# Performance work log

Hardware: AMD Instinct MI355X
Metric: run time of the kernel (lower is better)

Reference implementation:

```python
import jax, jax.numpy as jnp
import numpy as np

B, T, N, R, I = 32, 512, 1024, 4, 8
DT = 0.1
G = 0.9


def setup_inputs() -> dict:
    key = jax.random.key(0)
    k1, k2, k3, k4, k5 = jax.random.split(key, 5)
    inputs = jax.random.normal(k1, (B, T, I, 1), dtype=jnp.float32)
    f = jax.random.normal(k2, (B, T, R, 1), dtype=jnp.float32)
    J = jax.random.normal(k3, (B, N, N), dtype=jnp.float32) * (G / np.sqrt(N))
    wIn = jax.random.normal(k4, (B, N, I), dtype=jnp.float32)
    m = jax.random.normal(k5, (B, N, R), dtype=jnp.float32)
    return {"inputs": inputs, "f": f, "J": J, "wIn": wIn, "m": m}


def _run(inputs, f, J, wIn, m):
    dt = DT
    dtype = inputs.dtype
    x0 = jnp.zeros((B, N, 1), dtype)
    n0 = jnp.zeros((B, N, R), dtype)
    P0 = jnp.tile(jnp.eye(N, dtype=dtype)[None] / 10.0, (B, 1, 1))

    def step(carry, t_in):
        x, P, n = carry
        u, f_t = t_in                               # u: (B,I,1), f_t: (B,R,1)
        # recurrence (r, z computed from PRE-update x, matching original)
        r = jnp.tanh(x)                             # (B,N,1)
        z = jnp.einsum('bnk,bns->bks', n, r)        # n^T @ r -> (B,R,1)
        x_new = (1.0 - dt) * x + dt * (J @ r + m @ z + wIn @ u)
        # RLS update (uses r from pre-update x)
        Pr = P @ r                                  # (B,N,1)
        rPr = jnp.sum(r * Pr, axis=1, keepdims=True)  # r^T P r -> (B,1,1)
        c = 1.0 / (1.0 + rPr)                       # scalar per batch
        P_new = P - c * (Pr @ jnp.swapaxes(Pr, -1, -2))
        err = z - f_t                               # (B,R,1)
        n_new = n - c * (Pr @ jnp.swapaxes(err, -1, -2))
        return (x_new, P_new, n_new), (x_new, z)

    u_seq = jnp.swapaxes(inputs, 0, 1)              # (T,B,I,1)
    f_seq = jnp.swapaxes(f, 0, 1)                   # (T,B,R,1)
    _, (xs, zs) = jax.lax.scan(step, (x0, P0, n0), (u_seq, f_seq))
    all_x = jnp.swapaxes(xs, 0, 1)                  # (B,T,N,1)
    all_z = jnp.swapaxes(zs, 0, 1)                  # (B,T,R,1)
    return all_x, all_z


def reference(inputs, f, J, wIn, m):
    return _run(inputs, f, J, wIn, m)
```

## Files before the change

### kernel.cpp

```cpp
#include <hip/hip_runtime.h>
#include <hip/hip_bf16.h>

#define BB 32
#define TT 512
#define NN 1024
#define RR 4
#define II 8
#define DT_C 0.1f

#define BPB 32
#define GRID (BB * BPB)

#define NBLK 32
#define ROWS (NN / NBLK)
#define VBLK 16

typedef __attribute__((ext_vector_type(8))) unsigned short ushort8v;

__device__ __forceinline__ float bf2f(unsigned short u) {
    union { unsigned int ui; float f; } cv;
    cv.ui = ((unsigned int)u) << 16;
    return cv.f;
}
__device__ __forceinline__ unsigned short f2bf_rne(float x) {
    union { float f; unsigned int ui; } cv; cv.f = x;
    unsigned int u = cv.ui;
    u += 0x7FFFu + ((u >> 16) & 1u);
    return (unsigned short)(u >> 16);
}
__device__ __forceinline__ float wave_reduce(float v) {
    #pragma unroll
    for (int off = 32; off; off >>= 1) v += __shfl_down(v, off, 64);
    return v;
}

__device__ __forceinline__ void llc_ld16x2(const void* p0, const void* p1,
                                           uint4& a, uint4& b) {
    asm volatile("global_load_dwordx4 %0, %2, off sc0 sc1\n\t"
                 "global_load_dwordx4 %1, %3, off sc0 sc1\n\t"
                 "s_waitcnt vmcnt(0)"
                 : "=&v"(a), "=&v"(b) : "v"(p0), "v"(p1) : "memory");
}
__device__ __forceinline__ uint4 llc_ld16(const void* p) {
    uint4 r;
    asm volatile("global_load_dwordx4 %0, %1, off sc0 sc1\n\ts_waitcnt vmcnt(0)"
                 : "=&v"(r) : "v"(p) : "memory");
    return r;
}
__device__ __forceinline__ float llc_ldf(const float* p) {
    float r;
    asm volatile("global_load_dword %0, %1, off sc0 sc1\n\ts_waitcnt vmcnt(0)"
                 : "=&v"(r) : "v"(p) : "memory");
    return r;
}
__device__ __forceinline__ void llc_ld4f(const float* p0, const float* p1,
                                         const float* p2, const float* p3,
                                         float& a, float& b, float& c, float& d) {
    asm volatile("global_load_dword %0, %4, off sc0 sc1\n\t"
                 "global_load_dword %1, %5, off sc0 sc1\n\t"
                 "global_load_dword %2, %6, off sc0 sc1\n\t"
                 "global_load_dword %3, %7, off sc0 sc1\n\t"
                 "s_waitcnt vmcnt(0)"
                 : "=&v"(a), "=&v"(b), "=&v"(c), "=&v"(d)
                 : "v"(p0), "v"(p1), "v"(p2), "v"(p3) : "memory");
}
__device__ __forceinline__ void llc_stf(float* p, float v) {
    asm volatile("global_store_dword %0, %1, off sc0 sc1" :: "v"(p), "v"(v) : "memory");
}
__device__ __forceinline__ void llc_st16b(unsigned short* p, unsigned short v) {
    asm volatile("global_store_short %0, %1, off sc0 sc1"
                 :: "v"(p), "v"((unsigned)v) : "memory");
}

__device__ __forceinline__ void accum8(float& acc, const uint4 q, const float* ap) {
    acc = fmaf(bf2f((unsigned short)(q.x & 0xffffu)), ap[0], acc);
    acc = fmaf(bf2f((unsigned short)(q.x >> 16)),     ap[1], acc);
    acc = fmaf(bf2f((unsigned short)(q.y & 0xffffu)), ap[2], acc);
    acc = fmaf(bf2f((unsigned short)(q.y >> 16)),     ap[3], acc);
    acc = fmaf(bf2f((unsigned short)(q.z & 0xffffu)), ap[4], acc);
    acc = fmaf(bf2f((unsigned short)(q.z >> 16)),     ap[5], acc);
    acc = fmaf(bf2f((unsigned short)(q.w & 0xffffu)), ap[6], acc);
    acc = fmaf(bf2f((unsigned short)(q.w >> 16)),     ap[7], acc);
}


__global__ __launch_bounds__(256) void k_convJ(const float* __restrict__ J,
                                               unsigned short* __restrict__ Jp) {
    const int row = blockIdx.x;
    const int tid = threadIdx.x;
    __shared__ float rowsh[NN];
    const float4* __restrict__ src = (const float4*)(J + (size_t)row * NN);
    float4* dst4 = (float4*)rowsh;
    for (int k = tid; k < NN / 4; k += 256) dst4[k] = src[k];
    __syncthreads();
    const int o0 = tid * 4;
    unsigned short out[4];
    #pragma unroll
    for (int j = 0; j < 4; ++j) {
        const int o = o0 + j;
        const int l = (o >> 3) & 63, g = o >> 9, e = o & 7;
        out[j] = f2bf_rne(rowsh[l + 64 * (8 * g + e)]);
    }
    uint2 w;
    w.x = (unsigned int)out[0] | ((unsigned int)out[1] << 16);
    w.y = (unsigned int)out[2] | ((unsigned int)out[3] << 16);
    *(uint2*)(Jp + (size_t)row * NN + o0) = w;
}

__device__ __forceinline__ void batch_barrier(unsigned* cnt, unsigned* gen,
                                              unsigned expect) {
    asm volatile("s_waitcnt vmcnt(0) lgkmcnt(0)" ::: "memory");
    __syncthreads();
    if (threadIdx.x == 0) {
        unsigned old = __hip_atomic_fetch_add(cnt, 1u, __ATOMIC_RELAXED,
                                              __HIP_MEMORY_SCOPE_AGENT);
        if (old == BPB - 1u) {
            __hip_atomic_store(cnt, 0u, __ATOMIC_RELAXED, __HIP_MEMORY_SCOPE_AGENT);
            asm volatile("s_waitcnt vmcnt(0)" ::: "memory");
            __hip_atomic_fetch_add(gen, 1u, __ATOMIC_RELAXED, __HIP_MEMORY_SCOPE_AGENT);
        } else {
            while (__hip_atomic_load(gen, __ATOMIC_RELAXED, __HIP_MEMORY_SCOPE_AGENT)
                   < expect)
                __builtin_amdgcn_s_sleep(2);
        }
    }
    __syncthreads();
}

#define ACC2(q, base) \
    acc = fmaf(bf2f((unsigned short)((q) & 0xffffu)), r_sh[(base)], acc); \
    acc = fmaf(bf2f((unsigned short)((q) >> 16)), r_sh[(base) + 64], acc);

__global__ __launch_bounds__(256, 4) void k_persist(
    const unsigned short* __restrict__ Jp,
    unsigned short* __restrict__ V1,
    unsigned short* __restrict__ V2,
    float* __restrict__ x,
    float* __restrict__ abuf,
    float* __restrict__ part,
    float* __restrict__ part2,
    unsigned* __restrict__ cnt, unsigned* __restrict__ gen,
    const float* __restrict__ m, const float* __restrict__ wIn,
    const float* __restrict__ inputs, const float* __restrict__ f,
    float* __restrict__ outx, float* __restrict__ outz)
{
    const int bid = blockIdx.x;
    const int b = (bid & 7) * 4 + (bid >> 8);
    const int k = (bid >> 3) & 31;
    const int tid = threadIdx.x, lane = tid & 63, wave = tid >> 6;
    const int row_loc = tid >> 3, sub = tid & 7;
    const int i_loc = k * 32 + row_loc;

    __shared__ float r_sh[NN];
    __shared__ float a_sh[TT];
    __shared__ float Jr_sh[32];
    __shared__ float zred[32][4];
    __shared__ float red_neg[4], red_rr[4];
    __shared__ float sgred[33];
    __shared__ float zr2[128];
    __shared__ float zsh[RR], esh[RR], ush[II], csh[2];

    unsigned* mycnt = cnt + b * 32;
    unsigned* mygen = gen + b * 32;
    unsigned bar = 0;

    float4 nrow = {0.f, 0.f, 0.f, 0.f};
    float xreg = 0.f;

    for (int t = 0; t < TT; ++t) {
        {
            float x0, x1, x2, x3;
            const float* xb = x + b * NN + tid;
            llc_ld4f(xb, xb + 256, xb + 512, xb + 768, x0, x1, x2, x3);
            r_sh[tid]       = tanhf(x0);
            r_sh[tid + 256] = tanhf(x1);
            r_sh[tid + 512] = tanhf(x2);
            r_sh[tid + 768] = tanhf(x3);
        }
        __syncthreads();

        for (int rr = wave; rr < 32; rr += 4) {
            const int row = k * 32 + rr;
            const ushort8v* __restrict__ Jrow =
                (const ushort8v*)(Jp + ((size_t)b * NN + row) * NN);
            const ushort8v j0 = Jrow[lane];
            const ushort8v j1 = Jrow[64 + lane];
            float acc = 0.f;
            #pragma unroll
            for (int e = 0; e < 8; ++e)
                acc = fmaf(bf2f(j0[e]), r_sh[lane + 64 * e], acc);
            #pragma unroll
            for (int e = 0; e < 8; ++e)
                acc = fmaf(bf2f(j1[e]), r_sh[lane + 512 + 64 * e], acc);
            acc = wave_reduce(acc);
            if (lane == 0) Jr_sh[rr] = acc;
        }

        if (sub == 0) {
            const float rv = r_sh[i_loc];
            zred[row_loc][0] = nrow.x * rv;
            zred[row_loc][1] = nrow.y * rv;
            zred[row_loc][2] = nrow.z * rv;
            zred[row_loc][3] = nrow.w * rv;
        }

        float negsum = 0.f;
        for (int s = k + 32 * wave; s < t; s += 128) {
            const unsigned short* colp = V1 + ((size_t)b * TT + s) * NN;
            uint4 q0, q1;
            llc_ld16x2(colp + lane * 8, colp + (64 + lane) * 8, q0, q1);
            float acc = 0.f;
            ACC2(q0.x, lane);       ACC2(q0.y, lane + 128);
            ACC2(q0.z, lane + 256); ACC2(q0.w, lane + 384);
            ACC2(q1.x, lane + 512); ACC2(q1.y, lane + 640);
            ACC2(q1.z, lane + 768); ACC2(q1.w, lane + 896);
            acc = wave_reduce(acc);
            if (lane == 0) {
                llc_stf(abuf + b * TT + s, acc);
                negsum = fmaf(-acc, acc, negsum);
            }
        }
        if (lane == 0) red_neg[wave] = negsum;

        if (k == 0) {
            float p = 0.f;
            for (int j = tid; j < NN; j += 256) p = fmaf(r_sh[j], r_sh[j], p);
            p = wave_reduce(p);
            if (lane == 0) red_rr[wave] = p;
        }
        __syncthreads();
        if (tid < 4) {
            float zp = 0.f;
            #pragma unroll
            for (int kk = 0; kk < 32; ++kk) zp += zred[kk][tid];
            llc_stf(part2 + b * 128 + k * 4 + tid, zp);
        }
        if (tid == 0)
            llc_stf(part + b * 64 + k,
                    red_neg[0] + red_neg[1] + red_neg[2] + red_neg[3]);
        if (k == 0 && tid == 0)
            llc_stf(part + b * 64 + 32,
                    0.1f * (red_rr[0] + red_rr[1] + red_rr[2] + red_rr[3]));

        batch_barrier(mycnt, mygen, ++bar);

        const int nv4 = (t + 3) >> 2;
        if (tid < nv4) {
            union { uint4 u; float4 fv; } cv;
            cv.u = llc_ld16(abuf + b * TT + tid * 4);
            const int s0 = tid * 4;
            a_sh[s0]     = (s0     < t) ? cv.fv.x : 0.f;
            a_sh[s0 + 1] = (s0 + 1 < t) ? cv.fv.y : 0.f;
            a_sh[s0 + 2] = (s0 + 2 < t) ? cv.fv.z : 0.f;
            a_sh[s0 + 3] = (s0 + 3 < t) ? cv.fv.w : 0.f;
        }
        for (int j2 = nv4 * 4 + tid; j2 < TT; j2 += 256) a_sh[j2] = 0.f;
        if (tid < 33) sgred[tid] = llc_ldf(part + b * 64 + tid);
        if (tid >= 64 && tid < 192) zr2[tid - 64] = llc_ldf(part2 + b * 128 + (tid - 64));
        if (tid >= 192 && tid < 192 + II)
            ush[tid - 192] = inputs[((size_t)b * TT + t) * II + (tid - 192)];
        __syncthreads();
        if (tid == 0) {
            float sg = 0.f;
            #pragma unroll
            for (int q2 = 0; q2 < 33; ++q2) sg += sgred[q2];
            const float c = 1.f / (1.f + sg);
            csh[0] = c; csh[1] = sqrtf(c);
        }
        if (tid < 4) {
            float zq = 0.f;
            #pragma unroll
            for (int kk = 0; kk < 32; ++kk) zq += zr2[kk * 4 + tid];
            zsh[tid] = zq;
            esh[tid] = zq - f[((size_t)b * TT + t) * RR + tid];
        }
        __syncthreads();

        const unsigned short* vrow = V2 + ((size_t)b * NN + i_loc) * TT;
        const int nj = (t + 63) >> 6;
        float acc = 0.f;
        int j2 = 0;
        for (; j2 + 2 <= nj; j2 += 2) {
            uint4 qa, qb;
            const int o0 = j2 * 64 + sub * 8, o1 = o0 + 64;
            llc_ld16x2(vrow + o0, vrow + o1, qa, qb);
            accum8(acc, qa, a_sh + o0);
            accum8(acc, qb, a_sh + o1);
        }
        if (j2 < nj) {
            const int o0 = j2 * 64 + sub * 8;
            uint4 qa = llc_ld16(vrow + o0);
            accum8(acc, qa, a_sh + o0);
        }
        acc += __shfl_down(acc, 4, 8);
        acc += __shfl_down(acc, 2, 8);
        acc += __shfl_down(acc, 1, 8);

        if (sub == 0) {
            const float c = csh[0], sq = csh[1];
            const float pr = 0.1f * r_sh[i_loc] - acc;
            const unsigned short hv = f2bf_rne(sq * pr);
            const int ge = i_loc >> 6;
            const int o = (ge >> 3) * 512 + (i_loc & 63) * 8 + (ge & 7);
            llc_st16b(V1 + ((size_t)b * TT + t) * NN + o, hv);
            llc_st16b(V2 + ((size_t)b * NN + i_loc) * TT + t, hv);

            float accx = Jr_sh[row_loc];
            const float4 mv = *(const float4*)(m + ((size_t)b * NN + i_loc) * RR);
            accx = fmaf(mv.x, zsh[0], accx); accx = fmaf(mv.y, zsh[1], accx);
            accx = fmaf(mv.z, zsh[2], accx); accx = fmaf(mv.w, zsh[3], accx);
            const float4* __restrict__ wp =
                (const float4*)(wIn + ((size_t)b * NN + i_loc) * II);
            const float4 w0 = wp[0], w1 = wp[1];
            accx = fmaf(w0.x, ush[0], accx); accx = fmaf(w0.y, ush[1], accx);
            accx = fmaf(w0.z, ush[2], accx); accx = fmaf(w0.w, ush[3], accx);
            accx = fmaf(w1.x, ush[4], accx); accx = fmaf(w1.y, ush[5], accx);
            accx = fmaf(w1.z, ush[6], accx); accx = fmaf(w1.w, ush[7], accx);
            const float xn = (1.0f - DT_C) * xreg + DT_C * accx;
            xreg = xn;
            llc_stf(x + b * NN + i_loc, xn);
            outx[((size_t)b * TT + t) * NN + i_loc] = xn;

            const float cpr = c * pr;
            nrow.x = fmaf(-cpr, esh[0], nrow.x);
            nrow.y = fmaf(-cpr, esh[1], nrow.y);
            nrow.z = fmaf(-cpr, esh[2], nrow.z);
            nrow.w = fmaf(-cpr, esh[3], nrow.w);
        }
        if (k == 0 && tid < RR) outz[((size_t)b * TT + t) * RR + tid] = zsh[tid];

        batch_barrier(mycnt, mygen, ++bar);
    }
}


__global__ __launch_bounds__(256) void kA_fb(
    const float* __restrict__ x, const unsigned short* __restrict__ Jp,
    const unsigned short* __restrict__ Vp, const float* __restrict__ nmat,
    float* __restrict__ r_out, float* __restrict__ a_out,
    float* __restrict__ Jr, float* __restrict__ zbuf,
    float* __restrict__ part, int t)
{
    const int b   = blockIdx.x / (NBLK + VBLK);
    const int blk = blockIdx.x % (NBLK + VBLK);
    const int tid = threadIdx.x, lane = tid & 63, wave = tid >> 6;

    __shared__ float r_sh[NN];
    __shared__ float red_sh[4];

    for (int j = tid; j < NN; j += 256) {
        const float rv = tanhf(x[b * NN + j]);
        r_sh[j] = rv;
        if (blk == 0) r_out[b * NN + j] = rv;
    }
    __syncthreads();

    if (blk < NBLK) {
        for (int rr = wave; rr < ROWS; rr += 4) {
            const int row = blk * ROWS + rr;
            const ushort8v* __restrict__ Jrow =
                (const ushort8v*)(Jp + ((size_t)b * NN + row) * NN);
            const ushort8v jv0 = Jrow[lane];
            const ushort8v jv1 = Jrow[64 + lane];
            float acc = 0.0f;
            #pragma unroll
            for (int e = 0; e < 8; ++e) acc = fmaf(bf2f(jv0[e]), r_sh[lane + 64 * e], acc);
            #pragma unroll
            for (int e = 0; e < 8; ++e) acc = fmaf(bf2f(jv1[e]), r_sh[lane + 512 + 64 * e], acc);
            acc = wave_reduce(acc);
            if (lane == 0) Jr[b * NN + row] = acc;
        }
        if (blk == 0) {
            float p = 0.0f;
            for (int j = tid; j < NN; j += 256) p = fmaf(r_sh[j], r_sh[j], p);
            p = wave_reduce(p);
            if (lane == 0) red_sh[wave] = p;
            __syncthreads();
            if (tid == 0)
                part[b * 72 + 64] = 0.1f * (red_sh[0] + red_sh[1] + red_sh[2] + red_sh[3]);
            if (wave < RR) {
                float acc = 0.0f;
                for (int i2 = lane; i2 < NN; i2 += 64)
                    acc = fmaf(nmat[((size_t)b * NN + i2) * RR + wave], r_sh[i2], acc);
                acc = wave_reduce(acc);
                if (lane == 0) zbuf[b * RR + wave] = acc;
            }
        }
    } else {
        const int wid = (blk - NBLK) * 4 + wave;
        float negsum = 0.0f;
        for (int s = wid; s < t; s += 64) {
            const ushort8v* __restrict__ col =
                (const ushort8v*)(Vp + ((size_t)b * TT + s) * NN);
            const ushort8v vv0 = col[lane];
            const ushort8v vv1 = col[64 + lane];
            float acc = 0.0f;
            #pragma unroll
            for (int e = 0; e < 8; ++e) acc = fmaf(bf2f(vv0[e]), r_sh[lane + 64 * e], acc);
            #pragma unroll
            for (int e = 0; e < 8; ++e) acc = fmaf(bf2f(vv1[e]), r_sh[lane + 512 + 64 * e], acc);
            acc = wave_reduce(acc);
            if (lane == 0) {
                a_out[b * TT + s] = acc;
                negsum = fmaf(-acc, acc, negsum);
            }
        }
        if (lane == 0) part[b * 72 + wid] = negsum;
    }
}

__global__ __launch_bounds__(256) void kB_fb(
    unsigned short* __restrict__ Vp, const float* __restrict__ r,
    const float* __restrict__ a, const float* __restrict__ Jr,
    const float* __restrict__ zbuf, const float* __restrict__ part,
    float* __restrict__ x, float* __restrict__ nmat,
    const float* __restrict__ m, const float* __restrict__ wIn,
    const float* __restrict__ inputs, const float* __restrict__ f,
    float* __restrict__ outx, float* __restrict__ outz, int t)
{
    const int b   = blockIdx.x >> 3;
    const int tb  = blockIdx.x & 7;
    const int tid = threadIdx.x;
    const int pl    = tid & 63;
    const int slice = tid >> 6;

    __shared__ float a_sh[TT];
    __shared__ float ps[4][128];
    __shared__ float zsh[RR], esh[RR], ush[II];

    for (int s = tid; s < t; s += 256) a_sh[s] = a[b * TT + s];
    if (tid < RR) {
        const float zv = zbuf[b * RR + tid];
        zsh[tid] = zv;
        esh[tid] = zv - f[((size_t)b * TT + t) * RR + tid];
    }
    if (tid >= 64 && tid < 64 + II)
        ush[tid - 64] = inputs[((size_t)b * TT + t) * II + (tid - 64)];
    __syncthreads();

    const int p0 = (tb * 64 + pl) * 2;
    const unsigned short* __restrict__ Vb = Vp + (size_t)b * TT * NN;

    const int s_begin = (t * slice) >> 2;
    const int s_end   = (t * (slice + 1)) >> 2;
    float acc0 = 0.0f, acc1 = 0.0f;
    #pragma unroll 4
    for (int s = s_begin; s < s_end; ++s) {
        const unsigned int w = *(const unsigned int*)(Vb + (size_t)s * NN + p0);
        const float av = a_sh[s];
        acc0 = fmaf(bf2f((unsigned short)(w & 0xFFFFu)), av, acc0);
        acc1 = fmaf(bf2f((unsigned short)(w >> 16)), av, acc1);
    }
    ps[slice][pl * 2]     = acc0;
    ps[slice][pl * 2 + 1] = acc1;
    __syncthreads();

    if (slice == 0) {
        const int l = (p0 >> 3) & 63, g = p0 >> 9, e = p0 & 7;
        const int i0 = l + 64 * (8 * g + e);
        const int i1 = i0 + 64;
        const float s0 = ps[0][pl * 2] + ps[1][pl * 2] + ps[2][pl * 2] + ps[3][pl * 2];
        const float s1 = ps[0][pl * 2 + 1] + ps[1][pl * 2 + 1] + ps[2][pl * 2 + 1] + ps[3][pl * 2 + 1];

        float sg = 0.0f;
        #pragma unroll
        for (int q = 0; q < 65; ++q) sg += part[b * 72 + q];
        const float c  = 1.0f / (1.0f + sg);
        const float sq = sqrtf(c);

        const float pr0 = 0.1f * r[b * NN + i0] - s0;
        const float pr1 = 0.1f * r[b * NN + i1] - s1;

        unsigned int wv = (unsigned int)f2bf_rne(sq * pr0) |
                          ((unsigned int)f2bf_rne(sq * pr1) << 16);
        *(unsigned int*)(Vp + ((size_t)b * TT + t) * NN + p0) = wv;

        #pragma unroll
        for (int which = 0; which < 2; ++which) {
            const int   i  = which ? i1 : i0;
            const float pr = which ? pr1 : pr0;
            float acc = Jr[b * NN + i];
            const float4 mv = *(const float4*)(m + ((size_t)b * NN + i) * RR);
            acc = fmaf(mv.x, zsh[0], acc); acc = fmaf(mv.y, zsh[1], acc);
            acc = fmaf(mv.z, zsh[2], acc); acc = fmaf(mv.w, zsh[3], acc);
            const float4* __restrict__ wp = (const float4*)(wIn + ((size_t)b * NN + i) * II);
            const float4 w0 = wp[0], w1 = wp[1];
            acc = fmaf(w0.x, ush[0], acc); acc = fmaf(w0.y, ush[1], acc);
            acc = fmaf(w0.z, ush[2], acc); acc = fmaf(w0.w, ush[3], acc);
            acc = fmaf(w1.x, ush[4], acc); acc = fmaf(w1.y, ush[5], acc);
            acc = fmaf(w1.z, ush[6], acc); acc = fmaf(w1.w, ush[7], acc);
            const float xo = x[b * NN + i];
            const float xn = (1.0f - DT_C) * xo + DT_C * acc;
            x[b * NN + i] = xn;
            outx[((size_t)b * TT + t) * NN + i] = xn;

            float4* __restrict__ np = (float4*)(nmat + ((size_t)b * NN + i) * RR);
            float4 nv = *np;
            const float cpr = c * pr;
            nv.x = fmaf(-cpr, esh[0], nv.x); nv.y = fmaf(-cpr, esh[1], nv.y);
            nv.z = fmaf(-cpr, esh[2], nv.z); nv.w = fmaf(-cpr, esh[3], nv.w);
            *np = nv;
        }
    }
    if (tb == 0 && tid < RR) outz[((size_t)b * TT + t) * RR + tid] = zsh[tid];
}

extern "C" void kernel_launch(void* const* d_in, const int* in_sizes, int n_in,
                              void* d_out, int out_size, void* d_ws, size_t ws_size,
                              hipStream_t stream) {
    const float* inputs = (const float*)d_in[0];
    const float* f      = (const float*)d_in[1];
    const float* J      = (const float*)d_in[2];
    const float* wIn    = (const float*)d_in[3];
    const float* m      = (const float*)d_in[4];

    float* outx = (float*)d_out;
    float* outz = outx + (size_t)BB * TT * NN;

    char* ws = (char*)d_ws;
    size_t off = 0;
    unsigned short* Jp = (unsigned short*)(ws + off); off += (size_t)BB * NN * NN * 2;
    unsigned short* V1 = (unsigned short*)(ws + off); off += (size_t)BB * TT * NN * 2;
    unsigned short* V2 = (unsigned short*)(ws + off); off += (size_t)BB * NN * TT * 2;
    float* x      = (float*)(ws + off); off += (size_t)BB * NN * 4;
    float* abuf   = (float*)(ws + off); off += (size_t)BB * TT * 4;
    float* part   = (float*)(ws + off); off += (size_t)BB * 64 * 4;
    float* part2  = (float*)(ws + off); off += (size_t)BB * 128 * 4;
    unsigned* cnt = (unsigned*)(ws + off); off += (size_t)BB * 32 * 4;
    unsigned* gen = (unsigned*)(ws + off); off += (size_t)BB * 32 * 4;
    float* nm     = (float*)(ws + off); off += (size_t)BB * NN * RR * 4;
    float* rbuf   = (float*)(ws + off); off += (size_t)BB * NN * 4;
    float* Jrb    = (float*)(ws + off); off += (size_t)BB * NN * 4;
    float* zb     = (float*)(ws + off); off += (size_t)BB * RR * 4 + 256;
    float* part72 = (float*)(ws + off); off += (size_t)BB * 72 * 4;

    hipMemsetAsync(x,   0, (size_t)BB * NN * sizeof(float), stream);
    hipMemsetAsync(nm,  0, (size_t)BB * NN * RR * sizeof(float), stream);
    hipMemsetAsync(cnt, 0, (size_t)BB * 32 * sizeof(unsigned), stream);
    hipMemsetAsync(gen, 0, (size_t)BB * 32 * sizeof(unsigned), stream);

    k_convJ<<<BB * NN, 256, 0, stream>>>(J, Jp);

    void* kargs[] = {
        (void*)&Jp, (void*)&V1, (void*)&V2, (void*)&x,
        (void*)&abuf, (void*)&part, (void*)&part2, (void*)&cnt, (void*)&gen,
        (void*)&m, (void*)&wIn, (void*)&inputs, (void*)&f,
        (void*)&outx, (void*)&outz
    };
    hipError_t rc = hipLaunchCooperativeKernel((const void*)k_persist,
                                               dim3(GRID), dim3(256),
                                               kargs, 0, stream);
    if (rc != hipSuccess) {
        for (int t = 0; t < TT; ++t) {
            kA_fb<<<BB * (NBLK + VBLK), 256, 0, stream>>>(x, Jp, V1, nm, rbuf, abuf,
                                                          Jrb, zb, part72, t);
            kB_fb<<<BB * 8, 256, 0, stream>>>(V1, rbuf, abuf, Jrb, zb, part72,
                                              x, nm, m, wIn, inputs, f, outx, outz, t);
        }
    }
}
```

Measured before the change: 9.451 ms.

## Keep J slice in registers and V panel in LDS, reorder per-step partials

Each persistent block now loads its bf16 slice of J into 64 registers per thread once, instead of re-reading J rows from global memory every timestep. The low-rank V factors for the block's 32 rows are held in shared memory rather than in two global buffers. The projection partials for the next step are computed locally and exchanged through small global buffers. The intent is to remove the per-step global traffic for J and V. In exchange, register and LDS use rises sharply, which may lower occupancy or cause spills, and the barrier sequence per step is rearranged to use two batch barriers.

```diff
diff --git a/kernel.cpp b/kernel.cpp
--- a/kernel.cpp
+++ b/kernel.cpp
@@ -18,14 +18,17 @@
 typedef __attribute__((ext_vector_type(8))) unsigned short ushort8v;
 
 __device__ __forceinline__ float bf2f(unsigned short u) {
-    union { unsigned int ui; float f; } cv;
-    cv.ui = ((unsigned int)u) << 16;
-    return cv.f;
+    union { unsigned int ui; float f; } cv; cv.ui = ((unsigned int)u) << 16; return cv.f;
+}
+__device__ __forceinline__ float bf2f_lo(unsigned int u) {
+    union { unsigned int ui; float f; } cv; cv.ui = u << 16; return cv.f;
+}
+__device__ __forceinline__ float bf2f_hi(unsigned int u) {
+    union { unsigned int ui; float f; } cv; cv.ui = u & 0xffff0000u; return cv.f;
 }
 __device__ __forceinline__ unsigned short f2bf_rne(float x) {
     union { float f; unsigned int ui; } cv; cv.f = x;
-    unsigned int u = cv.ui;
-    u += 0x7FFFu + ((u >> 16) & 1u);
+    unsigned int u = cv.ui; u += 0x7FFFu + ((u >> 16) & 1u);
     return (unsigned short)(u >> 16);
 }
 __device__ __forceinline__ float wave_reduce(float v) {
@@ -34,13 +37,6 @@
     return v;
 }
 
-__device__ __forceinline__ void llc_ld16x2(const void* p0, const void* p1,
-                                           uint4& a, uint4& b) {
-    asm volatile("global_load_dwordx4 %0, %2, off sc0 sc1\n\t"
-                 "global_load_dwordx4 %1, %3, off sc0 sc1\n\t"
-                 "s_waitcnt vmcnt(0)"
-                 : "=&v"(a), "=&v"(b) : "v"(p0), "v"(p1) : "memory");
-}
 __device__ __forceinline__ uint4 llc_ld16(const void* p) {
     uint4 r;
     asm volatile("global_load_dwordx4 %0, %1, off sc0 sc1\n\ts_waitcnt vmcnt(0)"
@@ -53,58 +49,40 @@
                  : "=&v"(r) : "v"(p) : "memory");
     return r;
 }
-__device__ __forceinline__ void llc_ld4f(const float* p0, const float* p1,
-                                         const float* p2, const float* p3,
-                                         float& a, float& b, float& c, float& d) {
-    asm volatile("global_load_dword %0, %4, off sc0 sc1\n\t"
-                 "global_load_dword %1, %5, off sc0 sc1\n\t"
-                 "global_load_dword %2, %6, off sc0 sc1\n\t"
-                 "global_load_dword %3, %7, off sc0 sc1\n\t"
+__device__ __forceinline__ void llc_ldf2(const float* p0, const float* p1,
+                                         float& a, float& b) {
+    asm volatile("global_load_dword %0, %2, off sc0 sc1\n\t"
+                 "global_load_dword %1, %3, off sc0 sc1\n\t"
                  "s_waitcnt vmcnt(0)"
-                 : "=&v"(a), "=&v"(b), "=&v"(c), "=&v"(d)
-                 : "v"(p0), "v"(p1), "v"(p2), "v"(p3) : "memory");
+                 : "=&v"(a), "=&v"(b) : "v"(p0), "v"(p1) : "memory");
 }
 __device__ __forceinline__ void llc_stf(float* p, float v) {
     asm volatile("global_store_dword %0, %1, off sc0 sc1" :: "v"(p), "v"(v) : "memory");
 }
-__device__ __forceinline__ void llc_st16b(unsigned short* p, unsigned short v) {
-    asm volatile("global_store_short %0, %1, off sc0 sc1"
-                 :: "v"(p), "v"((unsigned)v) : "memory");
-}
-
-__device__ __forceinline__ void accum8(float& acc, const uint4 q, const float* ap) {
-    acc = fmaf(bf2f((unsigned short)(q.x & 0xffffu)), ap[0], acc);
-    acc = fmaf(bf2f((unsigned short)(q.x >> 16)),     ap[1], acc);
-    acc = fmaf(bf2f((unsigned short)(q.y & 0xffffu)), ap[2], acc);
-    acc = fmaf(bf2f((unsigned short)(q.y >> 16)),     ap[3], acc);
-    acc = fmaf(bf2f((unsigned short)(q.z & 0xffffu)), ap[4], acc);
-    acc = fmaf(bf2f((unsigned short)(q.z >> 16)),     ap[5], acc);
-    acc = fmaf(bf2f((unsigned short)(q.w & 0xffffu)), ap[6], acc);
-    acc = fmaf(bf2f((unsigned short)(q.w >> 16)),     ap[7], acc);
-}
-
-
-__global__ __launch_bounds__(256) void k_convJ(const float* __restrict__ J,
-                                               unsigned short* __restrict__ Jp) {
-    const int row = blockIdx.x;
-    const int tid = threadIdx.x;
-    __shared__ float rowsh[NN];
-    const float4* __restrict__ src = (const float4*)(J + (size_t)row * NN);
-    float4* dst4 = (float4*)rowsh;
-    for (int k = tid; k < NN / 4; k += 256) dst4[k] = src[k];
-    __syncthreads();
-    const int o0 = tid * 4;
-    unsigned short out[4];
+__device__ __forceinline__ void llc_st8(float* p, float a, float b) {
+    float2 v; v.x = a; v.y = b;
+    asm volatile("global_store_dwordx2 %0, %1, off sc0 sc1" :: "v"(p), "v"(v) : "memory");
+}
+
+__global__ __launch_bounds__(256) void k_convJl(const float* __restrict__ J,
+                                                unsigned int* __restrict__ Jl) {
+    const int b = blockIdx.x >> 5, k = blockIdx.x & 31;
+    const int w = threadIdx.x >> 6, l = threadIdx.x & 63;
+    unsigned int* dst = Jl + ((((size_t)(b * 32 + k) * 4 + w) * 64 + l) * 64);
     #pragma unroll
-    for (int j = 0; j < 4; ++j) {
-        const int o = o0 + j;
-        const int l = (o >> 3) & 63, g = o >> 9, e = o & 7;
-        out[j] = f2bf_rne(rowsh[l + 64 * (8 * g + e)]);
-    }
-    uint2 w;
-    w.x = (unsigned int)out[0] | ((unsigned int)out[1] << 16);
-    w.y = (unsigned int)out[2] | ((unsigned int)out[3] << 16);
-    *(uint2*)(Jp + (size_t)row * NN + o0) = w;
+    for (int j = 0; j < 8; ++j) {
+        const int row = k * 32 + w * 8 + j;
+        const float* __restrict__ Jrow = J + ((size_t)b * NN + row) * NN;
+        unsigned int out[8];
+        #pragma unroll
+        for (int e2 = 0; e2 < 8; ++e2) {
+            const int c0 = l + 128 * e2;
+            out[e2] = (unsigned int)f2bf_rne(Jrow[c0]) |
+                      ((unsigned int)f2bf_rne(Jrow[c0 + 64]) << 16);
+        }
+        *(uint4*)(dst + j * 8)     = make_uint4(out[0], out[1], out[2], out[3]);
+        *(uint4*)(dst + j * 8 + 4) = make_uint4(out[4], out[5], out[6], out[7]);
+    }
 }
 
 __device__ __forceinline__ void batch_barrier(unsigned* cnt, unsigned* gen,
@@ -127,18 +105,14 @@
     __syncthreads();
 }
 
-#define ACC2(q, base) \
-    acc = fmaf(bf2f((unsigned short)((q) & 0xffffu)), r_sh[(base)], acc); \
-    acc = fmaf(bf2f((unsigned short)((q) >> 16)), r_sh[(base) + 64], acc);
-
 __global__ __launch_bounds__(256, 4) void k_persist(
-    const unsigned short* __restrict__ Jp,
-    unsigned short* __restrict__ V1,
-    unsigned short* __restrict__ V2,
-    float* __restrict__ x,
+    const unsigned int* __restrict__ Jl,
+    float* __restrict__ rbuf,
     float* __restrict__ abuf,
-    float* __restrict__ part,
-    float* __restrict__ part2,
+    float* __restrict__ pa,
+    float* __restrict__ sqpart,
+    float* __restrict__ r2part,
+    float* __restrict__ zpart,
     unsigned* __restrict__ cnt, unsigned* __restrict__ gen,
     const float* __restrict__ m, const float* __restrict__ wIn,
     const float* __restrict__ inputs, const float* __restrict__ f,
@@ -151,159 +125,157 @@
     const int row_loc = tid >> 3, sub = tid & 7;
     const int i_loc = k * 32 + row_loc;
 
+    __shared__ unsigned short V_lds[32][512];
     __shared__ float r_sh[NN];
     __shared__ float a_sh[TT];
+    __shared__ float r_next[32];
     __shared__ float Jr_sh[32];
+    __shared__ float r2sh[32];
     __shared__ float zred[32][4];
-    __shared__ float red_neg[4], red_rr[4];
-    __shared__ float sgred[33];
-    __shared__ float zr2[128];
-    __shared__ float zsh[RR], esh[RR], ush[II], csh[2];
+    __shared__ float red4[4][16];
+    __shared__ float csh[2], zsh[RR], esh[RR], ush[II];
 
     unsigned* mycnt = cnt + b * 32;
     unsigned* mygen = gen + b * 32;
     unsigned bar = 0;
 
+    unsigned int jreg[64];
+    {
+        const uint4* jp = (const uint4*)(Jl +
+            ((((size_t)(b * 32 + k) * 4 + wave) * 64 + lane) * 64));
+        #pragma unroll
+        for (int q = 0; q < 16; ++q) {
+            uint4 v = jp[q];
+            jreg[q * 4] = v.x; jreg[q * 4 + 1] = v.y;
+            jreg[q * 4 + 2] = v.z; jreg[q * 4 + 3] = v.w;
+        }
+    }
+    {
+        unsigned long long* vz = (unsigned long long*)&V_lds[0][0];
+        for (int q = tid; q < 32 * 512 / 4; q += 256) vz[q] = 0ull;
+    }
     float4 nrow = {0.f, 0.f, 0.f, 0.f};
     float xreg = 0.f;
+    if (sub == 0) llc_stf(rbuf + b * NN + i_loc, 0.f);
+    if (tid < 4)  llc_stf(zpart + b * 128 + k * 4 + tid, 0.f);
+    if (tid == 4) llc_stf(r2part + b * 32 + k, 0.f);
+    batch_barrier(mycnt, mygen, ++bar);
 
     for (int t = 0; t < TT; ++t) {
         {
-            float x0, x1, x2, x3;
-            const float* xb = x + b * NN + tid;
-            llc_ld4f(xb, xb + 256, xb + 512, xb + 768, x0, x1, x2, x3);
-            r_sh[tid]       = tanhf(x0);
-            r_sh[tid + 256] = tanhf(x1);
-            r_sh[tid + 512] = tanhf(x2);
-            r_sh[tid + 768] = tanhf(x3);
-        }
+            const int s_off = tid & 15, kk = tid >> 4;
+            const int s = k * 16 + s_off;
+            float v = 0.f;
+            if (s < t) {
+                float v0, v1;
+                llc_ldf2(pa + ((size_t)b * 32 + kk) * TT + s,
+                         pa + ((size_t)b * 32 + kk + 16) * TT + s, v0, v1);
+                v = v0 + v1;
+            }
+            v += __shfl_down(v, 32, 64);
+            v += __shfl_down(v, 16, 64);
+            if ((tid & 63) < 16) red4[wave][s_off] = v;
+            __syncthreads();
+            if (tid < 16) {
+                float a = red4[0][tid] + red4[1][tid] + red4[2][tid] + red4[3][tid];
+                const int s2 = k * 16 + tid;
+                float sq = 0.f;
+                if (s2 < t) { llc_stf(abuf + b * TT + s2, a); sq = a * a; }
+                sq += __shfl_down(sq, 8, 16);
+                sq += __shfl_down(sq, 4, 16);
+                sq += __shfl_down(sq, 2, 16);
+                sq += __shfl_down(sq, 1, 16);
+                if (tid == 0) llc_stf(sqpart + b * 32 + k, sq);
+            }
+        }
+        batch_barrier(mycnt, mygen, ++bar);
+
+        {
+            union { uint4 u; float4 fv; } cv;
+            cv.u = llc_ld16(rbuf + b * NN + tid * 4);
+            *(float4*)&r_sh[tid * 4] = cv.fv;
+        }
+        if (tid < 128) {
+            const int s0 = tid * 4;
+            if (s0 < t) {
+                union { uint4 u; float4 fv; } cv;
+                cv.u = llc_ld16(abuf + b * TT + s0);
+                a_sh[s0]     = cv.fv.x;
+                a_sh[s0 + 1] = (s0 + 1 < t) ? cv.fv.y : 0.f;
+                a_sh[s0 + 2] = (s0 + 2 < t) ? cv.fv.z : 0.f;
+                a_sh[s0 + 3] = (s0 + 3 < t) ? cv.fv.w : 0.f;
+            } else {
+                *(float4*)&a_sh[s0] = make_float4(0.f, 0.f, 0.f, 0.f);
+            }
+        }
+        if (wave == 0) {
+            float v = (lane < 32) ? 0.1f * llc_ldf(r2part + b * 32 + lane)
+                                  : -llc_ldf(sqpart + b * 32 + (lane - 32));
+            v = wave_reduce(v);
+            if (lane == 0) {
+                const float c = 1.f / (1.f + v);
+                csh[0] = c; csh[1] = sqrtf(c);
+            }
+        } else if (wave == 1) {
+            float v0, v1;
+            llc_ldf2(zpart + b * 128 + lane, zpart + b * 128 + 64 + lane, v0, v1);
+            float v = v0 + v1;
+            v += __shfl_down(v, 32, 64);
+            v += __shfl_down(v, 16, 64);
+            v += __shfl_down(v, 8, 64);
+            v += __shfl_down(v, 4, 64);
+            if (lane < RR) {
+                zsh[lane] = v;
+                esh[lane] = v - f[((size_t)b * TT + t) * RR + lane];
+                if (k == 0) outz[((size_t)b * TT + t) * RR + lane] = v;
+            }
+        }
+        if (tid >= 128 && tid < 128 + II)
+            ush[tid - 128] = inputs[((size_t)b * TT + t) * II + (tid - 128)];
         __syncthreads();
 
-        for (int rr = wave; rr < 32; rr += 4) {
-            const int row = k * 32 + rr;
-            const ushort8v* __restrict__ Jrow =
-                (const ushort8v*)(Jp + ((size_t)b * NN + row) * NN);
-            const ushort8v j0 = Jrow[lane];
-            const ushort8v j1 = Jrow[64 + lane];
-            float acc = 0.f;
-            #pragma unroll
-            for (int e = 0; e < 8; ++e)
-                acc = fmaf(bf2f(j0[e]), r_sh[lane + 64 * e], acc);
-            #pragma unroll
-            for (int e = 0; e < 8; ++e)
-                acc = fmaf(bf2f(j1[e]), r_sh[lane + 512 + 64 * e], acc);
-            acc = wave_reduce(acc);
-            if (lane == 0) Jr_sh[rr] = acc;
-        }
-
-        if (sub == 0) {
-            const float rv = r_sh[i_loc];
-            zred[row_loc][0] = nrow.x * rv;
-            zred[row_loc][1] = nrow.y * rv;
-            zred[row_loc][2] = nrow.z * rv;
-            zred[row_loc][3] = nrow.w * rv;
-        }
-
-        float negsum = 0.f;
-        for (int s = k + 32 * wave; s < t; s += 128) {
-            const unsigned short* colp = V1 + ((size_t)b * TT + s) * NN;
-            uint4 q0, q1;
-            llc_ld16x2(colp + lane * 8, colp + (64 + lane) * 8, q0, q1);
-            float acc = 0.f;
-            ACC2(q0.x, lane);       ACC2(q0.y, lane + 128);
-            ACC2(q0.z, lane + 256); ACC2(q0.w, lane + 384);
-            ACC2(q1.x, lane + 512); ACC2(q1.y, lane + 640);
-            ACC2(q1.z, lane + 768); ACC2(q1.w, lane + 896);
-            acc = wave_reduce(acc);
-            if (lane == 0) {
-                llc_stf(abuf + b * TT + s, acc);
-                negsum = fmaf(-acc, acc, negsum);
-            }
-        }
-        if (lane == 0) red_neg[wave] = negsum;
-
-        if (k == 0) {
-            float p = 0.f;
-            for (int j = tid; j < NN; j += 256) p = fmaf(r_sh[j], r_sh[j], p);
-            p = wave_reduce(p);
-            if (lane == 0) red_rr[wave] = p;
-        }
+        float accJ[8] = {0.f, 0.f, 0.f, 0.f, 0.f, 0.f, 0.f, 0.f};
+        #pragma unroll
+        for (int e2 = 0; e2 < 8; ++e2) {
+            const float rv0 = r_sh[lane + 128 * e2];
+            const float rv1 = r_sh[lane + 128 * e2 + 64];
+            #pragma unroll
+            for (int j = 0; j < 8; ++j) {
+                const unsigned int w = jreg[j * 8 + e2];
+                accJ[j] = fmaf(bf2f_lo(w), rv0, accJ[j]);
+                accJ[j] = fmaf(bf2f_hi(w), rv1, accJ[j]);
+            }
+        }
+        #pragma unroll
+        for (int j = 0; j < 8; ++j) {
+            float v = wave_reduce(accJ[j]);
+            if (lane == 0) Jr_sh[wave * 8 + j] = v;
+        }
+
+        float accp = 0.f;
+        for (int mm = 0; mm * 64 < t; ++mm) {
+            const int s0 = mm * 64 + sub * 8;
+            const ushort8v vv = *(const ushort8v*)&V_lds[row_loc][s0];
+            const float4 a0 = *(const float4*)&a_sh[s0];
+            const float4 a1 = *(const float4*)&a_sh[s0 + 4];
+            accp = fmaf(bf2f(vv[0]), a0.x, accp);
+            accp = fmaf(bf2f(vv[1]), a0.y, accp);
+            accp = fmaf(bf2f(vv[2]), a0.z, accp);
+            accp = fmaf(bf2f(vv[3]), a0.w, accp);
+            accp = fmaf(bf2f(vv[4]), a1.x, accp);
+            accp = fmaf(bf2f(vv[5]), a1.y, accp);
+            accp = fmaf(bf2f(vv[6]), a1.z, accp);
+            accp = fmaf(bf2f(vv[7]), a1.w, accp);
+        }
+        accp += __shfl_down(accp, 4, 8);
+        accp += __shfl_down(accp, 2, 8);
+        accp += __shfl_down(accp, 1, 8);
         __syncthreads();
-        if (tid < 4) {
-            float zp = 0.f;
-            #pragma unroll
-            for (int kk = 0; kk < 32; ++kk) zp += zred[kk][tid];
-            llc_stf(part2 + b * 128 + k * 4 + tid, zp);
-        }
-        if (tid == 0)
-            llc_stf(part + b * 64 + k,
-                    red_neg[0] + red_neg[1] + red_neg[2] + red_neg[3]);
-        if (k == 0 && tid == 0)
-            llc_stf(part + b * 64 + 32,
-                    0.1f * (red_rr[0] + red_rr[1] + red_rr[2] + red_rr[3]));
-
-        batch_barrier(mycnt, mygen, ++bar);
-
-        const int nv4 = (t + 3) >> 2;
-        if (tid < nv4) {
-            union { uint4 u; float4 fv; } cv;
-            cv.u = llc_ld16(abuf + b * TT + tid * 4);
-            const int s0 = tid * 4;
-            a_sh[s0]     = (s0     < t) ? cv.fv.x : 0.f;
-            a_sh[s0 + 1] = (s0 + 1 < t) ? cv.fv.y : 0.f;
-            a_sh[s0 + 2] = (s0 + 2 < t) ? cv.fv.z : 0.f;
-            a_sh[s0 + 3] = (s0 + 3 < t) ? cv.fv.w : 0.f;
-        }
-        for (int j2 = nv4 * 4 + tid; j2 < TT; j2 += 256) a_sh[j2] = 0.f;
-        if (tid < 33) sgred[tid] = llc_ldf(part + b * 64 + tid);
-        if (tid >= 64 && tid < 192) zr2[tid - 64] = llc_ldf(part2 + b * 128 + (tid - 64));
-        if (tid >= 192 && tid < 192 + II)
-            ush[tid - 192] = inputs[((size_t)b * TT + t) * II + (tid - 192)];
-        __syncthreads();
-        if (tid == 0) {
-            float sg = 0.f;
-            #pragma unroll
-            for (int q2 = 0; q2 < 33; ++q2) sg += sgred[q2];
-            const float c = 1.f / (1.f + sg);
-            csh[0] = c; csh[1] = sqrtf(c);
-        }
-        if (tid < 4) {
-            float zq = 0.f;
-            #pragma unroll
-            for (int kk = 0; kk < 32; ++kk) zq += zr2[kk * 4 + tid];
-            zsh[tid] = zq;
-            esh[tid] = zq - f[((size_t)b * TT + t) * RR + tid];
-        }
-        __syncthreads();
-
-        const unsigned short* vrow = V2 + ((size_t)b * NN + i_loc) * TT;
-        const int nj = (t + 63) >> 6;
-        float acc = 0.f;
-        int j2 = 0;
-        for (; j2 + 2 <= nj; j2 += 2) {
-            uint4 qa, qb;
-            const int o0 = j2 * 64 + sub * 8, o1 = o0 + 64;
-            llc_ld16x2(vrow + o0, vrow + o1, qa, qb);
-            accum8(acc, qa, a_sh + o0);
-            accum8(acc, qb, a_sh + o1);
-        }
-        if (j2 < nj) {
-            const int o0 = j2 * 64 + sub * 8;
-            uint4 qa = llc_ld16(vrow + o0);
-            accum8(acc, qa, a_sh + o0);
-        }
-        acc += __shfl_down(acc, 4, 8);
-        acc += __shfl_down(acc, 2, 8);
-        acc += __shfl_down(acc, 1, 8);
 
         if (sub == 0) {
             const float c = csh[0], sq = csh[1];
-            const float pr = 0.1f * r_sh[i_loc] - acc;
-            const unsigned short hv = f2bf_rne(sq * pr);
-            const int ge = i_loc >> 6;
-            const int o = (ge >> 3) * 512 + (i_loc & 63) * 8 + (ge & 7);
-            llc_st16b(V1 + ((size_t)b * TT + t) * NN + o, hv);
-            llc_st16b(V2 + ((size_t)b * NN + i_loc) * TT + t, hv);
+            const float pr = 0.1f * r_sh[i_loc] - accp;
+            V_lds[row_loc][t] = f2bf_rne(sq * pr);
 
             float accx = Jr_sh[row_loc];
             const float4 mv = *(const float4*)(m + ((size_t)b * NN + i_loc) * RR);
@@ -318,7 +290,6 @@
             accx = fmaf(w1.z, ush[6], accx); accx = fmaf(w1.w, ush[7], accx);
             const float xn = (1.0f - DT_C) * xreg + DT_C * accx;
             xreg = xn;
-            llc_stf(x + b * NN + i_loc, xn);
             outx[((size_t)b * TT + t) * NN + i_loc] = xn;
 
             const float cpr = c * pr;
@@ -326,13 +297,66 @@
             nrow.y = fmaf(-cpr, esh[1], nrow.y);
             nrow.z = fmaf(-cpr, esh[2], nrow.z);
             nrow.w = fmaf(-cpr, esh[3], nrow.w);
-        }
-        if (k == 0 && tid < RR) outz[((size_t)b * TT + t) * RR + tid] = zsh[tid];
-
+
+            const float rp = tanhf(xn);
+            r_next[row_loc] = rp;
+            r2sh[row_loc] = rp * rp;
+            llc_stf(rbuf + b * NN + i_loc, rp);
+            ((float4*)zred)[row_loc] = make_float4(nrow.x * rp, nrow.y * rp,
+                                                   nrow.z * rp, nrow.w * rp);
+        }
+        __syncthreads();
+
+        if (tid < 4) {
+            float zp = 0.f;
+            #pragma unroll
+            for (int i = 0; i < 32; ++i) zp += zred[i][tid];
+            llc_stf(zpart + b * 128 + k * 4 + tid, zp);
+        } else if (tid == 4) {
+            float r2 = 0.f;
+            #pragma unroll
+            for (int i = 0; i < 32; ++i) r2 += r2sh[i];
+            llc_stf(r2part + b * 32 + k, r2);
+        }
+        if (t < TT - 1) {
+            const int s0 = 2 * tid;
+            if (s0 <= t) {
+                float a0 = 0.f, a1 = 0.f;
+                for (int i = 0; i < 32; ++i) {
+                    const unsigned int vv = *(const unsigned int*)&V_lds[i][s0];
+                    const float rv = r_next[i];
+                    a0 = fmaf(bf2f_lo(vv), rv, a0);
+                    a1 = fmaf(bf2f_hi(vv), rv, a1);
+                }
+                llc_st8(pa + ((size_t)b * 32 + k) * TT + s0, a0, a1);
+            }
+        }
         batch_barrier(mycnt, mygen, ++bar);
     }
 }
 
+__global__ __launch_bounds__(256) void k_convJ_old(const float* __restrict__ J,
+                                                   unsigned short* __restrict__ Jp) {
+    const int row = blockIdx.x;
+    const int tid = threadIdx.x;
+    __shared__ float rowsh[NN];
+    const float4* __restrict__ src = (const float4*)(J + (size_t)row * NN);
+    float4* dst4 = (float4*)rowsh;
+    for (int k = tid; k < NN / 4; k += 256) dst4[k] = src[k];
+    __syncthreads();
+    const int o0 = tid * 4;
+    unsigned short out[4];
+    #pragma unroll
+    for (int j = 0; j < 4; ++j) {
+        const int o = o0 + j;
+        const int l = (o >> 3) & 63, g = o >> 9, e = o & 7;
+        out[j] = f2bf_rne(rowsh[l + 64 * (8 * g + e)]);
+    }
+    uint2 w;
+    w.x = (unsigned int)out[0] | ((unsigned int)out[1] << 16);
+    w.y = (unsigned int)out[2] | ((unsigned int)out[3] << 16);
+    *(uint2*)(Jp + (size_t)row * NN + o0) = w;
+}
 
 __global__ __launch_bounds__(256) void kA_fb(
     const float* __restrict__ x, const unsigned short* __restrict__ Jp,
@@ -519,31 +543,34 @@
 
     char* ws = (char*)d_ws;
     size_t off = 0;
-    unsigned short* Jp = (unsigned short*)(ws + off); off += (size_t)BB * NN * NN * 2;
-    unsigned short* V1 = (unsigned short*)(ws + off); off += (size_t)BB * TT * NN * 2;
-    unsigned short* V2 = (unsigned short*)(ws + off); off += (size_t)BB * NN * TT * 2;
-    float* x      = (float*)(ws + off); off += (size_t)BB * NN * 4;
+    unsigned int* Jl = (unsigned int*)(ws + off);  off += (size_t)BB * NN * NN * 2;
+    unsigned short* Jp_fb = (unsigned short*)Jl;
+    unsigned short* V1_fb = (unsigned short*)(ws + off); off += (size_t)BB * TT * NN * 2;
+    float* pa     = (float*)(ws + off); off += (size_t)BB * 32 * TT * 4;
+    float* rbuf   = (float*)(ws + off); off += (size_t)BB * NN * 4;
     float* abuf   = (float*)(ws + off); off += (size_t)BB * TT * 4;
-    float* part   = (float*)(ws + off); off += (size_t)BB * 64 * 4;
-    float* part2  = (float*)(ws + off); off += (size_t)BB * 128 * 4;
+    float* sqpart = (float*)(ws + off); off += (size_t)BB * 32 * 4;
+    float* r2part = (float*)(ws + off); off += (size_t)BB * 32 * 4;
+    float* zpart  = (float*)(ws + off); off += (size_t)BB * 128 * 4;
     unsigned* cnt = (unsigned*)(ws + off); off += (size_t)BB * 32 * 4;
     unsigned* gen = (unsigned*)(ws + off); off += (size_t)BB * 32 * 4;
+    float* x_fb   = (float*)(ws + off); off += (size_t)BB * NN * 4;
     float* nm     = (float*)(ws + off); off += (size_t)BB * NN * RR * 4;
-    float* rbuf   = (float*)(ws + off); off += (size_t)BB * NN * 4;
     float* Jrb    = (float*)(ws + off); off += (size_t)BB * NN * 4;
     float* zb     = (float*)(ws + off); off += (size_t)BB * RR * 4 + 256;
     float* part72 = (float*)(ws + off); off += (size_t)BB * 72 * 4;
 
-    hipMemsetAsync(x,   0, (size_t)BB * NN * sizeof(float), stream);
-    hipMemsetAsync(nm,  0, (size_t)BB * NN * RR * sizeof(float), stream);
     hipMemsetAsync(cnt, 0, (size_t)BB * 32 * sizeof(unsigned), stream);
     hipMemsetAsync(gen, 0, (size_t)BB * 32 * sizeof(unsigned), stream);
-
-    k_convJ<<<BB * NN, 256, 0, stream>>>(J, Jp);
+    hipMemsetAsync(x_fb, 0, (size_t)BB * NN * sizeof(float), stream);
+    hipMemsetAsync(nm,  0, (size_t)BB * NN * RR * sizeof(float), stream);
+
+    k_convJl<<<BB * 32, 256, 0, stream>>>(J, Jl);
 
     void* kargs[] = {
-        (void*)&Jp, (void*)&V1, (void*)&V2, (void*)&x,
-        (void*)&abuf, (void*)&part, (void*)&part2, (void*)&cnt, (void*)&gen,
+        (void*)&Jl, (void*)&rbuf, (void*)&abuf, (void*)&pa,
+        (void*)&sqpart, (void*)&r2part, (void*)&zpart,
+        (void*)&cnt, (void*)&gen,
         (void*)&m, (void*)&wIn, (void*)&inputs, (void*)&f,
         (void*)&outx, (void*)&outz
     };
@@ -551,11 +578,12 @@
                                                dim3(GRID), dim3(256),
                                                kargs, 0, stream);
     if (rc != hipSuccess) {
+        k_convJ_old<<<BB * NN, 256, 0, stream>>>(J, Jp_fb);
         for (int t = 0; t < TT; ++t) {
-            kA_fb<<<BB * (NBLK + VBLK), 256, 0, stream>>>(x, Jp, V1, nm, rbuf, abuf,
-                                                          Jrb, zb, part72, t);
-            kB_fb<<<BB * 8, 256, 0, stream>>>(V1, rbuf, abuf, Jrb, zb, part72,
-                                              x, nm, m, wIn, inputs, f, outx, outz, t);
-        }
-    }
-}
+            kA_fb<<<BB * (NBLK + VBLK), 256, 0, stream>>>(x_fb, Jp_fb, V1_fb, nm,
+                                                          rbuf, abuf, Jrb, zb, part72, t);
+            kB_fb<<<BB * 8, 256, 0, stream>>>(V1_fb, rbuf, abuf, Jrb, zb, part72,
+                                              x_fb, nm, m, wIn, inputs, f, outx, outz, t);
+        }
+    }
+}
```

New measurement: 14.63 ms. 1.55x slower.
